# Performance work log

Hardware: AMD Instinct MI355X
Metric: run time of the kernel (lower is better)

The kernel has to match this reference:

```python
import jax, jax.numpy as jnp
import numpy as np

N, E, B = 50000, 800000, 128
IN, HID, OUT = 15, 256, 128
EPS = 1e-5


def setup_inputs() -> dict:
    key = jax.random.key(0)
    ks = jax.random.split(key, 16)
    x = jax.random.normal(ks[0], (N, IN), jnp.float32)
    edge_index = jax.random.randint(ks[1], (2, E), 0, N, jnp.int32)
    batch = jnp.sort(jax.random.randint(ks[2], (N,), 0, B, jnp.int32))
    w = lambda k, i, o: jax.random.normal(k, (i, o), jnp.float32) * (1.0 / np.sqrt(i))
    return {
        "x": x, "edge_index": edge_index, "batch": batch,
        "Wl1": w(ks[3], IN, HID), "Wr1": w(ks[4], IN, HID), "b1": jnp.zeros((HID,), jnp.float32),
        "g1": jnp.ones((HID,), jnp.float32), "bt1": jnp.zeros((HID,), jnp.float32),
        "Wl2": w(ks[5], HID, HID), "Wr2": w(ks[6], HID, HID), "b2": jnp.zeros((HID,), jnp.float32),
        "g2": jnp.ones((HID,), jnp.float32), "bt2": jnp.zeros((HID,), jnp.float32),
        "Wl3": w(ks[7], HID, HID), "Wr3": w(ks[8], HID, HID), "b3": jnp.zeros((HID,), jnp.float32),
        "g3": jnp.ones((HID,), jnp.float32), "bt3": jnp.zeros((HID,), jnp.float32),
        "Wl4": w(ks[9], HID, OUT), "Wr4": w(ks[10], HID, OUT), "b4": jnp.zeros((OUT,), jnp.float32),
        "g4": jnp.ones((OUT,), jnp.float32), "bt4": jnp.zeros((OUT,), jnp.float32),
    }


def _sage(x, src, dst, Wl, Wr, b):
    # mean-aggregate source-node features at each target, then two GEMMs
    msg = x[src]                                            # (E, d)
    agg = jax.ops.segment_sum(msg, dst, num_segments=N)     # (N, d)
    cnt = jax.ops.segment_sum(jnp.ones((src.shape[0],), x.dtype), dst, num_segments=N)
    mean = agg / jnp.clip(cnt, 1.0)[:, None]
    return mean @ Wl + x @ Wr + b


def _ln(x, g, b):
    mu = jnp.mean(x, axis=-1, keepdims=True)
    var = jnp.mean(jnp.square(x - mu), axis=-1, keepdims=True)
    return (x - mu) * jax.lax.rsqrt(var + EPS) * g + b


def reference(x, edge_index, batch,
              Wl1, Wr1, b1, g1, bt1,
              Wl2, Wr2, b2, g2, bt2,
              Wl3, Wr3, b3, g3, bt3,
              Wl4, Wr4, b4, g4, bt4):
    src, dst = edge_index[0], edge_index[1]
    gelu = lambda h: jax.nn.gelu(h, approximate=False)
    h = gelu(_ln(_sage(x, src, dst, Wl1, Wr1, b1), g1, bt1))
    h = gelu(_ln(_sage(h, src, dst, Wl2, Wr2, b2), g2, bt2))
    h = gelu(_ln(_sage(h, src, dst, Wl3, Wr3, b3), g3, bt3))
    h = gelu(_ln(_sage(h, src, dst, Wl4, Wr4, b4), g4, bt4))
    # global mean pool per patch
    s = jax.ops.segment_sum(h, batch, num_segments=B)        # (B, out)
    c = jax.ops.segment_sum(jnp.ones((N,), h.dtype), batch, num_segments=B)
    return s / jnp.clip(c, 1.0)[:, None]
```

## Files before the change

kernel.cpp:

```cpp
#include <hip/hip_runtime.h>
#include <math.h>

constexpr int Nn   = 50000;
constexpr int Ee   = 800000;
constexpr int Bb   = 128;
constexpr int INF  = 15;
constexpr int HID  = 256;
constexpr int OUTF = 128;

constexpr int NCB   = (Nn + 255) / 256;
constexpr int CHUNK = 4096;
constexpr int NB1   = (Ee + CHUNK - 1) / CHUNK;
constexpr int SCANN = NCB * NB1;

typedef __attribute__((ext_vector_type(8))) __bf16 bf16x8;
typedef __attribute__((ext_vector_type(4))) float  f32x4;

__device__ __forceinline__ float gelu_f(float v) {
    float s = fabsf(v) * 0.7071067811865475f;
    float t = __builtin_amdgcn_rcpf(fmaf(0.3275911f, s, 1.0f));
    float p = fmaf(fmaf(fmaf(fmaf(1.061405429f, t, -1.453152027f),
                             t, 1.421413741f), t, -0.284496736f), t, 0.254829592f) * t;
    float e = __expf(-s * s);
    float er = copysignf(1.0f - p * e, v);
    return 0.5f * v * (1.0f + er);
}

__device__ __forceinline__ unsigned short f2bf(float f) {
    union { float f; unsigned int u; } v; v.f = f;
    unsigned int r = v.u + 0x7fffu + ((v.u >> 16) & 1u);
    return (unsigned short)(r >> 16);
}

__device__ __forceinline__ float bflo(unsigned int p) { return __uint_as_float(p << 16); }
__device__ __forceinline__ float bfhi(unsigned int p) { return __uint_as_float(p & 0xffff0000u); }


__global__ void k_sortA(const int* __restrict__ dst, int* __restrict__ Gcnt) {
    __shared__ int cnt[NCB];
    int tid = threadIdx.x, blk = blockIdx.x;
    for (int i = tid; i < NCB; i += 256) cnt[i] = 0;
    __syncthreads();
    int base = blk * CHUNK;
    for (int i = 0; i < CHUNK; i += 256) {
        int e = base + i + tid;
        if (e < Ee) atomicAdd(&cnt[dst[e] >> 8], 1);
    }
    __syncthreads();
    for (int i = tid; i < NCB; i += 256) Gcnt[i * NB1 + blk] = cnt[i];
}

__global__ void k_gscan_partial(const int* __restrict__ in, int* __restrict__ partial, int n) {
    __shared__ int s[256];
    int tid = threadIdx.x, i = blockIdx.x * 256 + tid;
    s[tid] = (i < n) ? in[i] : 0;
    __syncthreads();
    for (int off = 128; off; off >>= 1) {
        if (tid < off) s[tid] += s[tid + off];
        __syncthreads();
    }
    if (tid == 0) partial[blockIdx.x] = s[0];
}

__global__ void k_gscan_mid(int* __restrict__ partial, int nb) {
    __shared__ int s[256];
    int tid = threadIdx.x;
    int v = (tid < nb) ? partial[tid] : 0;
    s[tid] = v;
    __syncthreads();
    for (int off = 1; off < 256; off <<= 1) {
        int t = (tid >= off) ? s[tid - off] : 0;
        __syncthreads();
        s[tid] += t;
        __syncthreads();
    }
    if (tid < nb) partial[tid] = s[tid] - v;
}

__global__ void k_gscan_final(const int* __restrict__ in, const int* __restrict__ partial,
                              int* __restrict__ out, int n) {
    __shared__ int s[256];
    int tid = threadIdx.x, i = blockIdx.x * 256 + tid;
    int v = (i < n) ? in[i] : 0;
    s[tid] = v;
    __syncthreads();
    for (int off = 1; off < 256; off <<= 1) {
        int t = (tid >= off) ? s[tid - off] : 0;
        __syncthreads();
        s[tid] += t;
        __syncthreads();
    }
    if (i < n) out[i] = s[tid] - v + partial[blockIdx.x];
}

__global__ void k_sortC(const int* __restrict__ dst, const int* __restrict__ srcv,
                        const int* __restrict__ Goff, unsigned int* __restrict__ pairs) {
    __shared__ int cur[NCB];
    int tid = threadIdx.x, blk = blockIdx.x;
    for (int i = tid; i < NCB; i += 256) cur[i] = Goff[i * NB1 + blk];
    __syncthreads();
    int base = blk * CHUNK;
    for (int i = 0; i < CHUNK; i += 256) {
        int e = base + i + tid;
        if (e < Ee) {
            int d = dst[e];
            int p = atomicAdd(&cur[d >> 8], 1);
            pairs[p] = ((unsigned int)(d & 255) << 16) | (unsigned int)srcv[e];
        }
    }
}

__global__ void k_sortD(const unsigned int* __restrict__ pairs, const int* __restrict__ Goff,
                        int* __restrict__ offs, int* __restrict__ srcs, float* __restrict__ invc) {
    __shared__ int fcnt[256];
    __shared__ int fbase[256];
    __shared__ int s[256];
    int tid = threadIdx.x, cb = blockIdx.x;
    int cbase = Goff[cb * NB1];
    int cend = (cb + 1 < NCB) ? Goff[(cb + 1) * NB1] : Ee;
    fcnt[tid] = 0;
    __syncthreads();
    for (int e = cbase + tid; e < cend; e += 256)
        atomicAdd(&fcnt[pairs[e] >> 16], 1);
    __syncthreads();
    int v = fcnt[tid];
    s[tid] = v;
    __syncthreads();
    for (int off = 1; off < 256; off <<= 1) {
        int t = (tid >= off) ? s[tid - off] : 0;
        __syncthreads();
        s[tid] += t;
        __syncthreads();
    }
    fbase[tid] = cbase + s[tid] - v;
    int node = cb * 256 + tid;
    if (node < Nn) {
        offs[node] = fbase[tid];
        invc[node] = 1.0f / (float)(v > 1 ? v : 1);
    }
    __syncthreads();
    fcnt[tid] = fbase[tid];
    __syncthreads();
    for (int e = cbase + tid; e < cend; e += 256) {
        unsigned int pv = pairs[e];
        int p = atomicAdd(&fcnt[pv >> 16], 1);
        srcs[p] = (int)(pv & 0xFFFFu);
    }
}

__global__ void k_bsearch(const int* __restrict__ batch, int* __restrict__ boff,
                          int* __restrict__ offs) {
    int b = threadIdx.x;
    if (b <= Bb) {
        int lo = 0, hi = Nn;
        while (lo < hi) {
            int mid = (lo + hi) >> 1;
            if (batch[mid] < b) lo = mid + 1; else hi = mid;
        }
        boff[b] = lo;
    }
    if (b == 0) offs[Nn] = Ee;
}


template <int NOUT>
__global__ void k_prepW(const float* __restrict__ Wl, const float* __restrict__ Wr,
                        uint4* __restrict__ outw) {
    constexpr int NT = NOUT / 16;
    int G = blockIdx.x * 256 + threadIdx.x;
    int per = 2 * NT * 64;
    int S = G / per, rem = G % per;
    int lane = rem & 63, sT = rem >> 6;
    int s = sT / NT, T = sT % NT;
    int q = lane >> 4, m = lane & 15;
    int k0 = S * 64 + s * 32 + q * 8;
    int nc = T * 16 + m;
    union { uint4 u; unsigned short h[8]; } pk;
#pragma unroll
    for (int j = 0; j < 8; j++) {
        int kk = k0 + j;
        float wv = (kk < 256) ? Wl[kk * NOUT + nc] : Wr[(kk - 256) * NOUT + nc];
        pk.h[j] = f2bf(wv);
    }
    outw[G] = pk.u;
}

__global__ void k_prepW1(const float* __restrict__ Wl, const float* __restrict__ Wr,
                         uint4* __restrict__ outw) {
    int G = blockIdx.x * 256 + threadIdx.x;
    int T = G >> 6, lane = G & 63;
    int q = lane >> 4, m = lane & 15;
    int nc = T * 16 + m;
    union { uint4 u; unsigned short h[8]; } pk;
#pragma unroll
    for (int j = 0; j < 8; j++) {
        int k = q * 8 + j;
        float wv;
        if (k < 15)       wv = Wl[k * HID + nc];
        else if (k == 15) wv = 0.0f;
        else if (k < 31)  wv = Wr[(k - 16) * HID + nc];
        else              wv = 0.0f;
        pk.h[j] = f2bf(wv);
    }
    outw[G] = pk.u;
}


__global__ void k_prep1(const float* __restrict__ x, const int* __restrict__ offs,
                        const int* __restrict__ srcs, const float* __restrict__ invc,
                        unsigned short* __restrict__ A1) {
    int node = blockIdx.x * 16 + (threadIdx.x >> 4);
    int f = threadIdx.x & 15;
    int s0 = offs[node], s1 = offs[node + 1];
    float acc = 0.0f;
    for (int i = s0; i < s1; i++) {
        int s = srcs[i];
        if (f < 15) acc += x[s * INF + f];
    }
    unsigned short mv = (f < 15) ? f2bf(acc * invc[node]) : (unsigned short)0;
    unsigned short xv = (f < 15) ? f2bf(x[(size_t)node * INF + f]) : (unsigned short)0;
    A1[(size_t)node * 32 + f] = mv;
    A1[(size_t)node * 32 + 16 + f] = xv;
}


__device__ __forceinline__ void acc8(float* a, uint4 v) {
    a[0] += bflo(v.x); a[1] += bfhi(v.x);
    a[2] += bflo(v.y); a[3] += bfhi(v.y);
    a[4] += bflo(v.z); a[5] += bfhi(v.z);
    a[6] += bflo(v.w); a[7] += bfhi(v.w);
}

__global__ void k_agg256_bf(const uint4* __restrict__ h4, const int* __restrict__ offs,
                            const int* __restrict__ srcs, const float* __restrict__ invc,
                            uint4* __restrict__ mean4) {
    int node = blockIdx.x * 4 + (threadIdx.x >> 6);
    int lane = threadIdx.x & 63;
    int sub = lane >> 5, q = lane & 31;
    int s0 = offs[node], s1 = offs[node + 1];
    int deg = s1 - s0;
    int dcap = deg < 64 ? deg : 64;
    int myidx = (lane < deg) ? srcs[s0 + lane] : 0;
    float a[8] = {};
    int i = 0;
    for (; i + 16 <= dcap; i += 16) {
        int sA = __shfl(myidx, i + sub);
        int sB = __shfl(myidx, i + 2 + sub);
        int sC = __shfl(myidx, i + 4 + sub);
        int sD = __shfl(myidx, i + 6 + sub);
        int sE = __shfl(myidx, i + 8 + sub);
        int sF = __shfl(myidx, i + 10 + sub);
        int sG = __shfl(myidx, i + 12 + sub);
        int sH = __shfl(myidx, i + 14 + sub);
        uint4 vA = h4[(size_t)sA * 32 + q];
        uint4 vB = h4[(size_t)sB * 32 + q];
        uint4 vC = h4[(size_t)sC * 32 + q];
        uint4 vD = h4[(size_t)sD * 32 + q];
        uint4 vE = h4[(size_t)sE * 32 + q];
        uint4 vF = h4[(size_t)sF * 32 + q];
        uint4 vG = h4[(size_t)sG * 32 + q];
        uint4 vH = h4[(size_t)sH * 32 + q];
        acc8(a, vA); acc8(a, vB); acc8(a, vC); acc8(a, vD);
        acc8(a, vE); acc8(a, vF); acc8(a, vG); acc8(a, vH);
    }
    if (i + 8 <= dcap) {
        int sA = __shfl(myidx, i + sub);
        int sB = __shfl(myidx, i + 2 + sub);
        int sC = __shfl(myidx, i + 4 + sub);
        int sD = __shfl(myidx, i + 6 + sub);
        uint4 vA = h4[(size_t)sA * 32 + q];
        uint4 vB = h4[(size_t)sB * 32 + q];
        uint4 vC = h4[(size_t)sC * 32 + q];
        uint4 vD = h4[(size_t)sD * 32 + q];
        acc8(a, vA); acc8(a, vB); acc8(a, vC); acc8(a, vD);
        i += 8;
    }
    if (i + 4 <= dcap) {
        int sA = __shfl(myidx, i + sub);
        int sB = __shfl(myidx, i + 2 + sub);
        uint4 vA = h4[(size_t)sA * 32 + q];
        uint4 vB = h4[(size_t)sB * 32 + q];
        acc8(a, vA); acc8(a, vB);
        i += 4;
    }
    if (i + 2 <= dcap) {
        int sA = __shfl(myidx, i + sub);
        uint4 vA = h4[(size_t)sA * 32 + q];
        acc8(a, vA);
        i += 2;
    }
    if (i < dcap && sub == 0) {
        int sA = __shfl(myidx, i);
        uint4 vA = h4[(size_t)sA * 32 + q];
        acc8(a, vA);
    }
    for (int j = 64; j + 1 < deg; j += 2) {
        int s = srcs[s0 + j + sub];
        uint4 v = h4[(size_t)s * 32 + q];
        acc8(a, v);
    }
    if (deg > 64 && ((deg - 64) & 1) && sub == 0) {
        int s = srcs[s1 - 1];
        uint4 v = h4[(size_t)s * 32 + q];
        acc8(a, v);
    }
#pragma unroll
    for (int j = 0; j < 8; j++) a[j] += __shfl_xor(a[j], 32);
    if (sub == 0) {
        float ic = invc[node];
        uint4 o;
        o.x = (unsigned int)f2bf(a[0] * ic) | ((unsigned int)f2bf(a[1] * ic) << 16);
        o.y = (unsigned int)f2bf(a[2] * ic) | ((unsigned int)f2bf(a[3] * ic) << 16);
        o.z = (unsigned int)f2bf(a[4] * ic) | ((unsigned int)f2bf(a[5] * ic) << 16);
        o.w = (unsigned int)f2bf(a[6] * ic) | ((unsigned int)f2bf(a[7] * ic) << 16);
        mean4[(size_t)node * 32 + q] = o;
    }
}


template <int NOUT, bool F32OUT>
__global__ __launch_bounds__(256) void k_gemm_mfma(
    const unsigned short* __restrict__ Am,
    const unsigned short* __restrict__ Ah,
    const uint4* __restrict__ Wfrag,
    const float* __restrict__ bias, const float* __restrict__ g,
    const float* __restrict__ bt, void* __restrict__ outp, int n) {
    constexpr int NT = NOUT / 16;
    constexpr int CT = NT / 4;
    constexpr int SROW = 33;
    __shared__ __align__(16) uint4 Abuf[32 * SROW];
    __shared__ float lnbuf[2][4][32];
    int tid = threadIdx.x;
    int w = tid >> 6, lane = tid & 63;
    int q = lane >> 4, m = lane & 15;
    int rowbase = blockIdx.x * 32;

    f32x4 acc[2][CT];
#pragma unroll
    for (int i = 0; i < 2; i++)
#pragma unroll
        for (int t = 0; t < CT; t++) acc[i][t] = (f32x4)0.f;

    union U { uint4 u; bf16x8 b; };
    U a[2], breg[3][CT];

    auto stage = [&](const unsigned short* A) {
        const uint4* Ag = (const uint4*)A + (size_t)rowbase * 32;
        uint4 v[4];
#pragma unroll
        for (int j = 0; j < 4; j++) {
            int c = j * 256 + tid;
            int row = c >> 5;
            v[j] = (rowbase + row < n) ? Ag[c] : make_uint4(0u, 0u, 0u, 0u);
        }
#pragma unroll
        for (int j = 0; j < 4; j++) {
            int c = j * 256 + tid;
            int row = c >> 5, kc = c & 31;
            Abuf[row * SROW + kc] = v[j];
        }
    };
    auto loadB = [&](int p, U* br) {
#pragma unroll
        for (int t = 0; t < CT; t++)
            br[t].u = Wfrag[(size_t)(p * NT + w * CT + t) * 64 + lane];
    };

    stage(Am);
    loadB(0, breg[0]);
    loadB(1, breg[1]);
    __syncthreads();

#pragma unroll
    for (int ph = 0; ph < 2; ph++) {
        if (ph == 1) {
            __syncthreads();
            stage(Ah);
            __syncthreads();
        }
#pragma unroll
        for (int pp = 0; pp < 8; pp++) {
            int p = ph * 8 + pp;
            if (p + 2 < 16) loadB(p + 2, breg[(p + 2) % 3]);
#pragma unroll
            for (int i = 0; i < 2; i++)
                a[i].u = Abuf[(i * 16 + m) * SROW + pp * 4 + q];
#pragma unroll
            for (int i = 0; i < 2; i++)
#pragma unroll
                for (int t = 0; t < CT; t++)
                    acc[i][t] = __builtin_amdgcn_mfma_f32_16x16x32_bf16(
                        a[i].b, breg[p % 3][t].b, acc[i][t], 0, 0, 0);
        }
    }

    int col0 = w * CT * 16;
    float bv[CT], gv[CT], btv[CT];
#pragma unroll
    for (int t = 0; t < CT; t++) {
        int c = col0 + t * 16 + m;
        bv[t] = bias[c]; gv[t] = g[c]; btv[t] = bt[c];
    }
#pragma unroll
    for (int i = 0; i < 2; i++) {
#pragma unroll
        for (int r = 0; r < 4; r++) {
            float s1 = 0.f, s2 = 0.f;
#pragma unroll
            for (int t = 0; t < CT; t++) {
                float v = acc[i][t][r] + bv[t];
                acc[i][t][r] = v;
                s1 += v; s2 += v * v;
            }
#pragma unroll
            for (int o = 1; o < 16; o <<= 1) {
                s1 += __shfl_xor(s1, o);
                s2 += __shfl_xor(s2, o);
            }
            if (m == 0) {
                int row = i * 16 + q * 4 + r;
                lnbuf[0][w][row] = s1;
                lnbuf[1][w][row] = s2;
            }
        }
    }
    __syncthreads();
#pragma unroll
    for (int i = 0; i < 2; i++) {
#pragma unroll
        for (int r = 0; r < 4; r++) {
            int rit = i * 16 + q * 4 + r;
            float ts1 = lnbuf[0][0][rit] + lnbuf[0][1][rit] + lnbuf[0][2][rit] + lnbuf[0][3][rit];
            float ts2 = lnbuf[1][0][rit] + lnbuf[1][1][rit] + lnbuf[1][2][rit] + lnbuf[1][3][rit];
            float mu  = ts1 * (1.0f / NOUT);
            float var = ts2 * (1.0f / NOUT) - mu * mu;
            float rs  = 1.0f / sqrtf(var + 1e-5f);
            int row = rowbase + rit;
            if (row < n) {
#pragma unroll
                for (int t = 0; t < CT; t++) {
                    int c = col0 + t * 16 + m;
                    float y = (acc[i][t][r] - mu) * rs * gv[t] + btv[t];
                    float res = gelu_f(y);
                    if (F32OUT) ((float*)outp)[(size_t)row * NOUT + c] = res;
                    else ((unsigned short*)outp)[(size_t)row * NOUT + c] = f2bf(res);
                }
            }
        }
    }
}


__global__ __launch_bounds__(256) void k_gemm_mfma1(
    const unsigned short* __restrict__ A1, const uint4* __restrict__ Wfrag,
    const float* __restrict__ bias, const float* __restrict__ g,
    const float* __restrict__ bt, unsigned short* __restrict__ outp, int n) {
    constexpr int NT = 16, CT = 4;
    __shared__ float lnbuf[2][4][64];
    int tid = threadIdx.x;
    int w = tid >> 6, lane = tid & 63;
    int q = lane >> 4, m = lane & 15;
    int rowbase = blockIdx.x * 64;

    union U { uint4 u; bf16x8 b; };
    U a[4], b[CT];
#pragma unroll
    for (int i = 0; i < 4; i++) {
        int row = rowbase + i * 16 + m;
        a[i].u = (row < n) ? *(const uint4*)(A1 + (size_t)row * 32 + q * 8)
                           : make_uint4(0u, 0u, 0u, 0u);
    }
#pragma unroll
    for (int t = 0; t < CT; t++)
        b[t].u = Wfrag[(size_t)(w * CT + t) * 64 + lane];

    f32x4 acc[4][CT];
#pragma unroll
    for (int i = 0; i < 4; i++)
#pragma unroll
        for (int t = 0; t < CT; t++)
            acc[i][t] = __builtin_amdgcn_mfma_f32_16x16x32_bf16(
                a[i].b, b[t].b, (f32x4)0.f, 0, 0, 0);

    int col0 = w * CT * 16;
    float bv[CT], gv[CT], btv[CT];
#pragma unroll
    for (int t = 0; t < CT; t++) {
        int c = col0 + t * 16 + m;
        bv[t] = bias[c]; gv[t] = g[c]; btv[t] = bt[c];
    }
#pragma unroll
    for (int i = 0; i < 4; i++) {
#pragma unroll
        for (int r = 0; r < 4; r++) {
            float s1 = 0.f, s2 = 0.f;
#pragma unroll
            for (int t = 0; t < CT; t++) {
                float v = acc[i][t][r] + bv[t];
                acc[i][t][r] = v;
                s1 += v; s2 += v * v;
            }
#pragma unroll
            for (int o = 1; o < 16; o <<= 1) {
                s1 += __shfl_xor(s1, o);
                s2 += __shfl_xor(s2, o);
            }
            if (m == 0) {
                int row = i * 16 + q * 4 + r;
                lnbuf[0][w][row] = s1;
                lnbuf[1][w][row] = s2;
            }
        }
    }
    __syncthreads();
#pragma unroll
    for (int i = 0; i < 4; i++) {
#pragma unroll
        for (int r = 0; r < 4; r++) {
            int rit = i * 16 + q * 4 + r;
            float ts1 = lnbuf[0][0][rit] + lnbuf[0][1][rit] + lnbuf[0][2][rit] + lnbuf[0][3][rit];
            float ts2 = lnbuf[1][0][rit] + lnbuf[1][1][rit] + lnbuf[1][2][rit] + lnbuf[1][3][rit];
            float mu  = ts1 * (1.0f / HID);
            float var = ts2 * (1.0f / HID) - mu * mu;
            float rs  = 1.0f / sqrtf(var + 1e-5f);
            int row = rowbase + rit;
            if (row < n) {
#pragma unroll
                for (int t = 0; t < CT; t++) {
                    int c = col0 + t * 16 + m;
                    float y = (acc[i][t][r] - mu) * rs * gv[t] + btv[t];
                    outp[(size_t)row * HID + c] = f2bf(gelu_f(y));
                }
            }
        }
    }
}


__global__ __launch_bounds__(1024) void k_pool(const float* __restrict__ h,
                                               const int* __restrict__ boff,
                                               float* __restrict__ out) {
    __shared__ float red[8][128];
    int b = blockIdx.x, tid = threadIdx.x;
    int j = tid & 127, grp = tid >> 7;
    int s0 = boff[b], s1 = boff[b + 1];
    float a0 = 0.f, a1 = 0.f, a2 = 0.f, a3 = 0.f;
    int i = s0 + grp;
    for (; i + 24 < s1; i += 32) {
        a0 += h[(size_t)i * OUTF + j];
        a1 += h[(size_t)(i + 8) * OUTF + j];
        a2 += h[(size_t)(i + 16) * OUTF + j];
        a3 += h[(size_t)(i + 24) * OUTF + j];
    }
    for (; i < s1; i += 8) a0 += h[(size_t)i * OUTF + j];
    red[grp][j] = (a0 + a1) + (a2 + a3);
    __syncthreads();
    if (tid < 128) {
        float s = ((red[0][tid] + red[1][tid]) + (red[2][tid] + red[3][tid]))
                + ((red[4][tid] + red[5][tid]) + (red[6][tid] + red[7][tid]));
        int c = s1 - s0;
        out[b * OUTF + tid] = s / fmaxf((float)c, 1.0f);
    }
}


extern "C" void kernel_launch(void* const* d_in, const int* in_sizes, int n_in,
                              void* d_out, int out_size, void* d_ws, size_t ws_size,
                              hipStream_t stream) {
    const float* x     = (const float*)d_in[0];
    const int*   ei    = (const int*)d_in[1];
    const int*   src   = ei;
    const int*   dst   = ei + Ee;
    const int*   batch = (const int*)d_in[2];
    const float* Wl1 = (const float*)d_in[3];
    const float* Wr1 = (const float*)d_in[4];
    const float* b1  = (const float*)d_in[5];
    const float* g1  = (const float*)d_in[6];
    const float* bt1 = (const float*)d_in[7];
    const float* Wl2 = (const float*)d_in[8];
    const float* Wr2 = (const float*)d_in[9];
    const float* b2  = (const float*)d_in[10];
    const float* g2  = (const float*)d_in[11];
    const float* bt2 = (const float*)d_in[12];
    const float* Wl3 = (const float*)d_in[13];
    const float* Wr3 = (const float*)d_in[14];
    const float* b3  = (const float*)d_in[15];
    const float* g3  = (const float*)d_in[16];
    const float* bt3 = (const float*)d_in[17];
    const float* Wl4 = (const float*)d_in[18];
    const float* Wr4 = (const float*)d_in[19];
    const float* b4  = (const float*)d_in[20];
    const float* g4  = (const float*)d_in[21];
    const float* bt4 = (const float*)d_in[22];
    float* out = (float*)d_out;

    char* ws = (char*)d_ws;
    size_t off = 0;
    auto alloc = [&](size_t bytes) -> char* {
        char* p = ws + off;
        off = (off + bytes + 255) & ~(size_t)255;
        return p;
    };
    int*   offs    = (int*)alloc((size_t)(Nn + 1) * 4);
    int*   srcs    = (int*)alloc((size_t)Ee * 4);
    float* invc    = (float*)alloc((size_t)Nn * 4);
    int*   boff    = (int*)alloc((size_t)(Bb + 1) * 4);
    unsigned int* pairs = (unsigned int*)alloc((size_t)Ee * 4);
    int*   Gcnt    = (int*)alloc((size_t)SCANN * 4);
    int*   Goff    = (int*)alloc((size_t)SCANN * 4);
    int*   partial = (int*)alloc(256 * 4);
    unsigned short* A1    = (unsigned short*)alloc((size_t)Nn * 32 * 2);
    unsigned short* meanb = (unsigned short*)alloc((size_t)Nn * HID * 2);
    unsigned short* hA    = (unsigned short*)alloc((size_t)Nn * HID * 2);
    unsigned short* hB    = (unsigned short*)alloc((size_t)Nn * HID * 2);
    float* hOut    = (float*)alloc((size_t)Nn * OUTF * 4);
    uint4* W1f     = (uint4*)alloc((size_t)32 * HID * 2);
    uint4* W2f     = (uint4*)alloc((size_t)512 * HID * 2);
    uint4* W3f     = (uint4*)alloc((size_t)512 * HID * 2);
    uint4* W4f     = (uint4*)alloc((size_t)512 * OUTF * 2);

    int nbScan = (SCANN + 255) / 256;
    k_sortA<<<NB1, 256, 0, stream>>>(dst, Gcnt);
    k_gscan_partial<<<nbScan, 256, 0, stream>>>(Gcnt, partial, SCANN);
    k_gscan_mid<<<1, 256, 0, stream>>>(partial, nbScan);
    k_gscan_final<<<nbScan, 256, 0, stream>>>(Gcnt, partial, Goff, SCANN);
    k_sortC<<<NB1, 256, 0, stream>>>(dst, src, Goff, pairs);
    k_sortD<<<NCB, 256, 0, stream>>>(pairs, Goff, offs, srcs, invc);
    k_bsearch<<<1, 256, 0, stream>>>(batch, boff, offs);

    k_prepW1<<<4, 256, 0, stream>>>(Wl1, Wr1, W1f);
    k_prepW<256><<<64, 256, 0, stream>>>(Wl2, Wr2, W2f);
    k_prepW<256><<<64, 256, 0, stream>>>(Wl3, Wr3, W3f);
    k_prepW<128><<<32, 256, 0, stream>>>(Wl4, Wr4, W4f);

    int gb64 = (Nn + 63) / 64;
    int gb32 = (Nn + 31) / 32;
    k_prep1<<<Nn / 16, 256, 0, stream>>>(x, offs, srcs, invc, A1);
    k_gemm_mfma1<<<gb64, 256, 0, stream>>>(A1, W1f, b1, g1, bt1, hA, Nn);
    k_agg256_bf<<<Nn / 4, 256, 0, stream>>>((const uint4*)hA, offs, srcs, invc, (uint4*)meanb);
    k_gemm_mfma<256, false><<<gb32, 256, 0, stream>>>(meanb, hA, W2f, b2, g2, bt2, hB, Nn);
    k_agg256_bf<<<Nn / 4, 256, 0, stream>>>((const uint4*)hB, offs, srcs, invc, (uint4*)meanb);
    k_gemm_mfma<256, false><<<gb32, 256, 0, stream>>>(meanb, hB, W3f, b3, g3, bt3, hA, Nn);
    k_agg256_bf<<<Nn / 4, 256, 0, stream>>>((const uint4*)hA, offs, srcs, invc, (uint4*)meanb);
    k_gemm_mfma<128, true><<<gb32, 256, 0, stream>>>(meanb, hA, W4f, b4, g4, bt4, hOut, Nn);
    k_pool<<<Bb, 1024, 0, stream>>>(hOut, boff, out);
}
```

Measured before the change: 458.7 us.

## Fuse neighbor mean aggregation into SAGE GEMM kernel via shared memory

Each GEMM block of 32 rows now gathers and averages neighbor features for its own rows straight into the shared A buffer, instead of a separate aggregation kernel writing a bf16 mean buffer to global memory. This removes three kernel launches and the write and read-back of the N×256 mean tensor per layer. In exchange each block does 8 sequential node gathers per wave before the MFMA phase, with fewer waves in flight for the latency-bound gather and no overlap between gather and compute.

```diff
diff --git a/kernel.cpp b/kernel.cpp
--- a/kernel.cpp
+++ b/kernel.cpp
@@ -231,97 +231,11 @@
     a[6] += bflo(v.w); a[7] += bfhi(v.w);
 }
 
-__global__ void k_agg256_bf(const uint4* __restrict__ h4, const int* __restrict__ offs,
-                            const int* __restrict__ srcs, const float* __restrict__ invc,
-                            uint4* __restrict__ mean4) {
-    int node = blockIdx.x * 4 + (threadIdx.x >> 6);
-    int lane = threadIdx.x & 63;
-    int sub = lane >> 5, q = lane & 31;
-    int s0 = offs[node], s1 = offs[node + 1];
-    int deg = s1 - s0;
-    int dcap = deg < 64 ? deg : 64;
-    int myidx = (lane < deg) ? srcs[s0 + lane] : 0;
-    float a[8] = {};
-    int i = 0;
-    for (; i + 16 <= dcap; i += 16) {
-        int sA = __shfl(myidx, i + sub);
-        int sB = __shfl(myidx, i + 2 + sub);
-        int sC = __shfl(myidx, i + 4 + sub);
-        int sD = __shfl(myidx, i + 6 + sub);
-        int sE = __shfl(myidx, i + 8 + sub);
-        int sF = __shfl(myidx, i + 10 + sub);
-        int sG = __shfl(myidx, i + 12 + sub);
-        int sH = __shfl(myidx, i + 14 + sub);
-        uint4 vA = h4[(size_t)sA * 32 + q];
-        uint4 vB = h4[(size_t)sB * 32 + q];
-        uint4 vC = h4[(size_t)sC * 32 + q];
-        uint4 vD = h4[(size_t)sD * 32 + q];
-        uint4 vE = h4[(size_t)sE * 32 + q];
-        uint4 vF = h4[(size_t)sF * 32 + q];
-        uint4 vG = h4[(size_t)sG * 32 + q];
-        uint4 vH = h4[(size_t)sH * 32 + q];
-        acc8(a, vA); acc8(a, vB); acc8(a, vC); acc8(a, vD);
-        acc8(a, vE); acc8(a, vF); acc8(a, vG); acc8(a, vH);
-    }
-    if (i + 8 <= dcap) {
-        int sA = __shfl(myidx, i + sub);
-        int sB = __shfl(myidx, i + 2 + sub);
-        int sC = __shfl(myidx, i + 4 + sub);
-        int sD = __shfl(myidx, i + 6 + sub);
-        uint4 vA = h4[(size_t)sA * 32 + q];
-        uint4 vB = h4[(size_t)sB * 32 + q];
-        uint4 vC = h4[(size_t)sC * 32 + q];
-        uint4 vD = h4[(size_t)sD * 32 + q];
-        acc8(a, vA); acc8(a, vB); acc8(a, vC); acc8(a, vD);
-        i += 8;
-    }
-    if (i + 4 <= dcap) {
-        int sA = __shfl(myidx, i + sub);
-        int sB = __shfl(myidx, i + 2 + sub);
-        uint4 vA = h4[(size_t)sA * 32 + q];
-        uint4 vB = h4[(size_t)sB * 32 + q];
-        acc8(a, vA); acc8(a, vB);
-        i += 4;
-    }
-    if (i + 2 <= dcap) {
-        int sA = __shfl(myidx, i + sub);
-        uint4 vA = h4[(size_t)sA * 32 + q];
-        acc8(a, vA);
-        i += 2;
-    }
-    if (i < dcap && sub == 0) {
-        int sA = __shfl(myidx, i);
-        uint4 vA = h4[(size_t)sA * 32 + q];
-        acc8(a, vA);
-    }
-    for (int j = 64; j + 1 < deg; j += 2) {
-        int s = srcs[s0 + j + sub];
-        uint4 v = h4[(size_t)s * 32 + q];
-        acc8(a, v);
-    }
-    if (deg > 64 && ((deg - 64) & 1) && sub == 0) {
-        int s = srcs[s1 - 1];
-        uint4 v = h4[(size_t)s * 32 + q];
-        acc8(a, v);
-    }
-#pragma unroll
-    for (int j = 0; j < 8; j++) a[j] += __shfl_xor(a[j], 32);
-    if (sub == 0) {
-        float ic = invc[node];
-        uint4 o;
-        o.x = (unsigned int)f2bf(a[0] * ic) | ((unsigned int)f2bf(a[1] * ic) << 16);
-        o.y = (unsigned int)f2bf(a[2] * ic) | ((unsigned int)f2bf(a[3] * ic) << 16);
-        o.z = (unsigned int)f2bf(a[4] * ic) | ((unsigned int)f2bf(a[5] * ic) << 16);
-        o.w = (unsigned int)f2bf(a[6] * ic) | ((unsigned int)f2bf(a[7] * ic) << 16);
-        mean4[(size_t)node * 32 + q] = o;
-    }
-}
-
-
 template <int NOUT, bool F32OUT>
-__global__ __launch_bounds__(256) void k_gemm_mfma(
-    const unsigned short* __restrict__ Am,
+__global__ __launch_bounds__(256) void k_fused(
     const unsigned short* __restrict__ Ah,
+    const int* __restrict__ offs, const int* __restrict__ srcs,
+    const float* __restrict__ invc,
     const uint4* __restrict__ Wfrag,
     const float* __restrict__ bias, const float* __restrict__ g,
     const float* __restrict__ bt, void* __restrict__ outp, int n) {
@@ -335,14 +249,111 @@
     int q = lane >> 4, m = lane & 15;
     int rowbase = blockIdx.x * 32;
 
+    union U { uint4 u; bf16x8 b; };
+    U a2[2], breg[3][CT];
+
+    auto loadB = [&](int p, U* br) {
+#pragma unroll
+        for (int t = 0; t < CT; t++)
+            br[t].u = Wfrag[(size_t)(p * NT + w * CT + t) * 64 + lane];
+    };
+    loadB(0, breg[0]);
+    loadB(1, breg[1]);
+
+    {
+        const uint4* h4 = (const uint4*)Ah;
+        int sub = lane >> 5, ql = lane & 31;
+        for (int jn = 0; jn < 8; jn++) {
+            int node = rowbase + w * 8 + jn;
+            float a[8] = {};
+            if (node < n) {
+                int s0 = offs[node], s1 = offs[node + 1];
+                int deg = s1 - s0;
+                int dcap = deg < 64 ? deg : 64;
+                int myidx = (lane < deg) ? srcs[s0 + lane] : 0;
+                int i = 0;
+                for (; i + 16 <= dcap; i += 16) {
+                    int sA = __shfl(myidx, i + sub);
+                    int sB = __shfl(myidx, i + 2 + sub);
+                    int sC = __shfl(myidx, i + 4 + sub);
+                    int sD = __shfl(myidx, i + 6 + sub);
+                    int sE = __shfl(myidx, i + 8 + sub);
+                    int sF = __shfl(myidx, i + 10 + sub);
+                    int sG = __shfl(myidx, i + 12 + sub);
+                    int sH = __shfl(myidx, i + 14 + sub);
+                    uint4 vA = h4[(size_t)sA * 32 + ql];
+                    uint4 vB = h4[(size_t)sB * 32 + ql];
+                    uint4 vC = h4[(size_t)sC * 32 + ql];
+                    uint4 vD = h4[(size_t)sD * 32 + ql];
+                    uint4 vE = h4[(size_t)sE * 32 + ql];
+                    uint4 vF = h4[(size_t)sF * 32 + ql];
+                    uint4 vG = h4[(size_t)sG * 32 + ql];
+                    uint4 vH = h4[(size_t)sH * 32 + ql];
+                    acc8(a, vA); acc8(a, vB); acc8(a, vC); acc8(a, vD);
+                    acc8(a, vE); acc8(a, vF); acc8(a, vG); acc8(a, vH);
+                }
+                if (i + 8 <= dcap) {
+                    int sA = __shfl(myidx, i + sub);
+                    int sB = __shfl(myidx, i + 2 + sub);
+                    int sC = __shfl(myidx, i + 4 + sub);
+                    int sD = __shfl(myidx, i + 6 + sub);
+                    uint4 vA = h4[(size_t)sA * 32 + ql];
+                    uint4 vB = h4[(size_t)sB * 32 + ql];
+                    uint4 vC = h4[(size_t)sC * 32 + ql];
+                    uint4 vD = h4[(size_t)sD * 32 + ql];
+                    acc8(a, vA); acc8(a, vB); acc8(a, vC); acc8(a, vD);
+                    i += 8;
+                }
+                if (i + 4 <= dcap) {
+                    int sA = __shfl(myidx, i + sub);
+                    int sB = __shfl(myidx, i + 2 + sub);
+                    uint4 vA = h4[(size_t)sA * 32 + ql];
+                    uint4 vB = h4[(size_t)sB * 32 + ql];
+                    acc8(a, vA); acc8(a, vB);
+                    i += 4;
+                }
+                if (i + 2 <= dcap) {
+                    int sA = __shfl(myidx, i + sub);
+                    uint4 vA = h4[(size_t)sA * 32 + ql];
+                    acc8(a, vA);
+                    i += 2;
+                }
+                if (i < dcap && sub == 0) {
+                    int sA = __shfl(myidx, i);
+                    uint4 vA = h4[(size_t)sA * 32 + ql];
+                    acc8(a, vA);
+                }
+                for (int j = 64; j + 1 < deg; j += 2) {
+                    int s = srcs[s0 + j + sub];
+                    uint4 v = h4[(size_t)s * 32 + ql];
+                    acc8(a, v);
+                }
+                if (deg > 64 && ((deg - 64) & 1) && sub == 0) {
+                    int s = srcs[s1 - 1];
+                    uint4 v = h4[(size_t)s * 32 + ql];
+                    acc8(a, v);
+                }
+            }
+#pragma unroll
+            for (int j = 0; j < 8; j++) a[j] += __shfl_xor(a[j], 32);
+            if (sub == 0) {
+                float ic = (node < n) ? invc[node] : 0.0f;
+                uint4 o;
+                o.x = (unsigned int)f2bf(a[0] * ic) | ((unsigned int)f2bf(a[1] * ic) << 16);
+                o.y = (unsigned int)f2bf(a[2] * ic) | ((unsigned int)f2bf(a[3] * ic) << 16);
+                o.z = (unsigned int)f2bf(a[4] * ic) | ((unsigned int)f2bf(a[5] * ic) << 16);
+                o.w = (unsigned int)f2bf(a[6] * ic) | ((unsigned int)f2bf(a[7] * ic) << 16);
+                Abuf[(w * 8 + jn) * SROW + ql] = o;
+            }
+        }
+    }
+    __syncthreads();
+
     f32x4 acc[2][CT];
 #pragma unroll
     for (int i = 0; i < 2; i++)
 #pragma unroll
         for (int t = 0; t < CT; t++) acc[i][t] = (f32x4)0.f;
-
-    union U { uint4 u; bf16x8 b; };
-    U a[2], breg[3][CT];
 
     auto stage = [&](const unsigned short* A) {
         const uint4* Ag = (const uint4*)A + (size_t)rowbase * 32;
@@ -360,16 +371,6 @@
             Abuf[row * SROW + kc] = v[j];
         }
     };
-    auto loadB = [&](int p, U* br) {
-#pragma unroll
-        for (int t = 0; t < CT; t++)
-            br[t].u = Wfrag[(size_t)(p * NT + w * CT + t) * 64 + lane];
-    };
-
-    stage(Am);
-    loadB(0, breg[0]);
-    loadB(1, breg[1]);
-    __syncthreads();
 
 #pragma unroll
     for (int ph = 0; ph < 2; ph++) {
@@ -384,13 +385,13 @@
             if (p + 2 < 16) loadB(p + 2, breg[(p + 2) % 3]);
 #pragma unroll
             for (int i = 0; i < 2; i++)
-                a[i].u = Abuf[(i * 16 + m) * SROW + pp * 4 + q];
+                a2[i].u = Abuf[(i * 16 + m) * SROW + pp * 4 + q];
 #pragma unroll
             for (int i = 0; i < 2; i++)
 #pragma unroll
                 for (int t = 0; t < CT; t++)
                     acc[i][t] = __builtin_amdgcn_mfma_f32_16x16x32_bf16(
-                        a[i].b, breg[p % 3][t].b, acc[i][t], 0, 0, 0);
+                        a2[i].b, breg[p % 3][t].b, acc[i][t], 0, 0, 0);
         }
     }
 
@@ -610,7 +611,6 @@
     int*   Goff    = (int*)alloc((size_t)SCANN * 4);
     int*   partial = (int*)alloc(256 * 4);
     unsigned short* A1    = (unsigned short*)alloc((size_t)Nn * 32 * 2);
-    unsigned short* meanb = (unsigned short*)alloc((size_t)Nn * HID * 2);
     unsigned short* hA    = (unsigned short*)alloc((size_t)Nn * HID * 2);
     unsigned short* hB    = (unsigned short*)alloc((size_t)Nn * HID * 2);
     float* hOut    = (float*)alloc((size_t)Nn * OUTF * 4);
@@ -637,11 +637,8 @@
     int gb32 = (Nn + 31) / 32;
     k_prep1<<<Nn / 16, 256, 0, stream>>>(x, offs, srcs, invc, A1);
     k_gemm_mfma1<<<gb64, 256, 0, stream>>>(A1, W1f, b1, g1, bt1, hA, Nn);
-    k_agg256_bf<<<Nn / 4, 256, 0, stream>>>((const uint4*)hA, offs, srcs, invc, (uint4*)meanb);
-    k_gemm_mfma<256, false><<<gb32, 256, 0, stream>>>(meanb, hA, W2f, b2, g2, bt2, hB, Nn);
-    k_agg256_bf<<<Nn / 4, 256, 0, stream>>>((const uint4*)hB, offs, srcs, invc, (uint4*)meanb);
-    k_gemm_mfma<256, false><<<gb32, 256, 0, stream>>>(meanb, hB, W3f, b3, g3, bt3, hA, Nn);
-    k_agg256_bf<<<Nn / 4, 256, 0, stream>>>((const uint4*)hA, offs, srcs, invc, (uint4*)meanb);
-    k_gemm_mfma<128, true><<<gb32, 256, 0, stream>>>(meanb, hA, W4f, b4, g4, bt4, hOut, Nn);
+    k_fused<256, false><<<gb32, 256, 0, stream>>>(hA, offs, srcs, invc, W2f, b2, g2, bt2, hB, Nn);
+    k_fused<256, false><<<gb32, 256, 0, stream>>>(hB, offs, srcs, invc, W3f, b3, g3, bt3, hA, Nn);
+    k_fused<128, true><<<gb32, 256, 0, stream>>>(hA, offs, srcs, invc, W4f, b4, g4, bt4, hOut, Nn);
     k_pool<<<Bb, 1024, 0, stream>>>(hOut, boff, out);
 }
```

Result: slower. 523.4 us (+14.1%).

## Pipeline aggregation and GEMM across node chunks in a fused mixed kernel

Applied to the files above, without the earlier changes.

Each SAGE layer's node range is split into four chunks. A combined kernel runs the aggregation of chunk c in its first blocks and the GEMM+LayerNorm of chunk c-1 in the rest, so the memory-bound gather overlaps with the MFMA GEMM on the GPU. This raises the number of launches per layer from two to five. Every block also carries the GEMM kernel's shared-memory and register footprint even when it only aggregates, which may reduce occupancy for the gather. Correctness holds because launches on one stream are serialized, so chunk c-1's means are complete before its GEMM runs.

```diff
diff --git a/kernel.cpp b/kernel.cpp
--- a/kernel.cpp
+++ b/kernel.cpp
@@ -12,6 +12,8 @@
 constexpr int CHUNK = 4096;
 constexpr int NB1   = (Ee + CHUNK - 1) / CHUNK;
 constexpr int SCANN = NCB * NB1;
+
+constexpr int S1 = 12512, S2 = 25024, S3 = 37536;
 
 typedef __attribute__((ext_vector_type(8))) __bf16 bf16x8;
 typedef __attribute__((ext_vector_type(4))) float  f32x4;
@@ -231,11 +233,12 @@
     a[6] += bflo(v.w); a[7] += bfhi(v.w);
 }
 
-__global__ void k_agg256_bf(const uint4* __restrict__ h4, const int* __restrict__ offs,
-                            const int* __restrict__ srcs, const float* __restrict__ invc,
-                            uint4* __restrict__ mean4) {
-    int node = blockIdx.x * 4 + (threadIdx.x >> 6);
-    int lane = threadIdx.x & 63;
+__device__ __forceinline__ void agg_node(const uint4* __restrict__ h4,
+                                         const int* __restrict__ offs,
+                                         const int* __restrict__ srcs,
+                                         const float* __restrict__ invc,
+                                         uint4* __restrict__ mean4,
+                                         int node, int lane) {
     int sub = lane >> 5, q = lane & 31;
     int s0 = offs[node], s1 = offs[node + 1];
     int deg = s1 - s0;
@@ -319,21 +322,33 @@
 
 
 template <int NOUT, bool F32OUT>
-__global__ __launch_bounds__(256) void k_gemm_mfma(
-    const unsigned short* __restrict__ Am,
+__global__ __launch_bounds__(256) void k_mix(
     const unsigned short* __restrict__ Ah,
+    const int* __restrict__ offs, const int* __restrict__ srcs,
+    const float* __restrict__ invc,
+    unsigned short* __restrict__ meanb,
     const uint4* __restrict__ Wfrag,
     const float* __restrict__ bias, const float* __restrict__ g,
-    const float* __restrict__ bt, void* __restrict__ outp, int n) {
+    const float* __restrict__ bt, void* __restrict__ outp, int n,
+    int aggN0, int aggN1, int gemmR0, int aggBlocks) {
     constexpr int NT = NOUT / 16;
     constexpr int CT = NT / 4;
     constexpr int SROW = 33;
     __shared__ __align__(16) uint4 Abuf[32 * SROW];
     __shared__ float lnbuf[2][4][32];
     int tid = threadIdx.x;
-    int w = tid >> 6, lane = tid & 63;
+    int lane = tid & 63;
+
+    if ((int)blockIdx.x < aggBlocks) {
+        int node = aggN0 + blockIdx.x * 4 + (tid >> 6);
+        if (node < aggN1)
+            agg_node((const uint4*)Ah, offs, srcs, invc, (uint4*)meanb, node, lane);
+        return;
+    }
+
+    int w = tid >> 6;
     int q = lane >> 4, m = lane & 15;
-    int rowbase = blockIdx.x * 32;
+    int rowbase = gemmR0 + ((int)blockIdx.x - aggBlocks) * 32;
 
     f32x4 acc[2][CT];
 #pragma unroll
@@ -342,7 +357,7 @@
         for (int t = 0; t < CT; t++) acc[i][t] = (f32x4)0.f;
 
     union U { uint4 u; bf16x8 b; };
-    U a[2], breg[3][CT];
+    U a2[2], breg[3][CT];
 
     auto stage = [&](const unsigned short* A) {
         const uint4* Ag = (const uint4*)A + (size_t)rowbase * 32;
@@ -366,7 +381,7 @@
             br[t].u = Wfrag[(size_t)(p * NT + w * CT + t) * 64 + lane];
     };
 
-    stage(Am);
+    stage(meanb);
     loadB(0, breg[0]);
     loadB(1, breg[1]);
     __syncthreads();
@@ -384,13 +399,13 @@
             if (p + 2 < 16) loadB(p + 2, breg[(p + 2) % 3]);
 #pragma unroll
             for (int i = 0; i < 2; i++)
-                a[i].u = Abuf[(i * 16 + m) * SROW + pp * 4 + q];
+                a2[i].u = Abuf[(i * 16 + m) * SROW + pp * 4 + q];
 #pragma unroll
             for (int i = 0; i < 2; i++)
 #pragma unroll
                 for (int t = 0; t < CT; t++)
                     acc[i][t] = __builtin_amdgcn_mfma_f32_16x16x32_bf16(
-                        a[i].b, breg[p % 3][t].b, acc[i][t], 0, 0, 0);
+                        a2[i].b, breg[p % 3][t].b, acc[i][t], 0, 0, 0);
         }
     }
 
@@ -634,14 +649,31 @@
     k_prepW<128><<<32, 256, 0, stream>>>(Wl4, Wr4, W4f);
 
     int gb64 = (Nn + 63) / 64;
-    int gb32 = (Nn + 31) / 32;
     k_prep1<<<Nn / 16, 256, 0, stream>>>(x, offs, srcs, invc, A1);
     k_gemm_mfma1<<<gb64, 256, 0, stream>>>(A1, W1f, b1, g1, bt1, hA, Nn);
-    k_agg256_bf<<<Nn / 4, 256, 0, stream>>>((const uint4*)hA, offs, srcs, invc, (uint4*)meanb);
-    k_gemm_mfma<256, false><<<gb32, 256, 0, stream>>>(meanb, hA, W2f, b2, g2, bt2, hB, Nn);
-    k_agg256_bf<<<Nn / 4, 256, 0, stream>>>((const uint4*)hB, offs, srcs, invc, (uint4*)meanb);
-    k_gemm_mfma<256, false><<<gb32, 256, 0, stream>>>(meanb, hB, W3f, b3, g3, bt3, hA, Nn);
-    k_agg256_bf<<<Nn / 4, 256, 0, stream>>>((const uint4*)hA, offs, srcs, invc, (uint4*)meanb);
-    k_gemm_mfma<128, true><<<gb32, 256, 0, stream>>>(meanb, hA, W4f, b4, g4, bt4, hOut, Nn);
+
+    const int bnd[5] = {0, S1, S2, S3, Nn};
+    auto aggB  = [&](int i) { return (bnd[i + 1] - bnd[i] + 3) / 4; };
+    auto gemmB = [&](int i) { return (bnd[i + 1] - bnd[i] + 31) / 32; };
+
+#define LAYER_PIPE(NOUTV, F32V, HIN, WF, BV, GV, BTV, HOUT)                              \
+    {                                                                                    \
+        k_mix<NOUTV, F32V><<<aggB(0), 256, 0, stream>>>(                                 \
+            HIN, offs, srcs, invc, meanb, WF, BV, GV, BTV, HOUT, Nn,                     \
+            bnd[0], bnd[1], 0, aggB(0));                                                 \
+        for (int c = 1; c < 4; c++)                                                      \
+            k_mix<NOUTV, F32V><<<aggB(c) + gemmB(c - 1), 256, 0, stream>>>(              \
+                HIN, offs, srcs, invc, meanb, WF, BV, GV, BTV, HOUT, Nn,                 \
+                bnd[c], bnd[c + 1], bnd[c - 1], aggB(c));                                \
+        k_mix<NOUTV, F32V><<<gemmB(3), 256, 0, stream>>>(                                \
+            HIN, offs, srcs, invc, meanb, WF, BV, GV, BTV, HOUT, Nn,                     \
+            0, 0, bnd[3], 0);                                                            \
+    }
+
+    LAYER_PIPE(256, false, hA, W2f, b2, g2, bt2, hB)
+    LAYER_PIPE(256, false, hB, W3f, b3, g3, bt3, hA)
+    LAYER_PIPE(128, true,  hA, W4f, b4, g4, bt4, hOut)
+#undef LAYER_PIPE
+
     k_pool<<<Bb, 1024, 0, stream>>>(hOut, boff, out);
 }
```

After: 557.8 us. +21.6%, slower.
